# Performance work log

Hardware: AMD Instinct MI355X
Metric: run time of the kernel (lower is better)

Reference implementation:

```python
import jax, jax.numpy as jnp
import numpy as np


def _block(x, W, b, use_relu):
    # x: (B, n, dx). Faithful to PairwiseInteractions: full pairwise L2 dist,
    # top-k (k == n) smallest sorted, drop self, concat(self, neighbor), linear,
    # optional relu, mean over the n-1 neighbors.
    B, n, dx = x.shape
    sq = jnp.sum(x * x, axis=-1)                                   # (B, n)
    d2 = sq[:, :, None] + sq[:, None, :] - 2.0 * jnp.einsum('bnd,bmd->bnm', x, x)
    dist = jnp.sqrt(jnp.maximum(d2, 0.0))                          # (B, n, n)
    _, idx = jax.lax.top_k(-dist, n)                               # ascending distances
    idx_nb = idx[:, :, 1:]                                         # drop self -> (B, n, n-1)
    nbr = jnp.take_along_axis(x[:, None, :, :], idx_nb[..., None], axis=2)  # (B, n, n-1, dx)
    self_rep = jnp.broadcast_to(x[:, :, None, :], nbr.shape)
    pairs = jnp.concatenate([self_rep, nbr], axis=-1)              # (B, n, n-1, 2*dx)
    h = pairs @ W + b
    if use_relu:
        h = jax.nn.relu(h)
    return jnp.sum(h, axis=2) / (n - 1)                            # (B, n, d_out)


def setup_inputs() -> dict:
    key = jax.random.key(0)
    ks = jax.random.split(key, 4)
    B, N, d = 2, 1024, 3

    def lin(k, fin, fout):
        kw, kb = jax.random.split(k)
        lim = 1.0 / np.sqrt(fin).astype(np.float32)
        W = jax.random.uniform(kw, (fin, fout), minval=-lim, maxval=lim, dtype=jnp.float32)
        b = jax.random.uniform(kb, (fout,), minval=-lim, maxval=lim, dtype=jnp.float32)
        return W, b

    W1, b1 = lin(ks[1], 2 * d, 32)
    W2, b2 = lin(ks[2], 2 * 32, 64)
    W3, b3 = lin(ks[3], 2 * 64, d)
    x = jax.random.normal(ks[0], (B, N * d), dtype=jnp.float32)
    return {"x": x, "W1": W1, "b1": b1, "W2": W2, "b2": b2, "W3": W3, "b3": b3}


def reference(x, W1, b1, W2, b2, W3, b3):
    B = x.shape[0]
    d = W3.shape[1]
    N = x.shape[1] // d
    h = x.reshape(B, N, d)
    h = _block(h, W1, b1, True)    # eb1: d -> 32, relu
    h = _block(h, W2, b2, True)    # eb2: 32 -> 64, relu
    h = _block(h, W3, b3, False)   # eb3: 64 -> d, no relu
    return h.reshape(B, N * d)
```

## Files before the change

### kernel.cpp

```cpp
#include <hip/hip_runtime.h>

#define NN 1024

__global__ __launch_bounds__(256) void k1_pair32_ac2(
    const float* __restrict__ x,  const float* __restrict__ W1, const float* __restrict__ b1,
    const float* __restrict__ W2, const float* __restrict__ b2,
    float* __restrict__ a2g, float* __restrict__ c2g)
{
    __shared__ float cbuf[8192];
    __shared__ float rowbuf[4][32];

    const int tid  = threadIdx.x;
    const int wave = tid >> 6, lane = tid & 63;
    const int blk  = blockIdx.x;

    const int i  = blk * 4 + wave;
    const int b  = i >> 10;
    const int il = i & 1023;
    const int js = lane >> 5, f = lane & 31;
    const float* xb = x + b * (NN * 3);

    const float xi0 = xb[il*3+0], xi1 = xb[il*3+1], xi2 = xb[il*3+2];
    const float a     = xi0*W1[0*32+f] + xi1*W1[1*32+f] + xi2*W1[2*32+f];
    const float cself = xi0*W1[3*32+f] + xi1*W1[4*32+f] + xi2*W1[5*32+f] + b1[f];

    float acc = 0.f;
    const int f2 = tid & 31, r0 = tid >> 5;
    const float w3f = W1[3*32+f2], w4f = W1[4*32+f2], w5f = W1[5*32+f2], bf = b1[f2];
    for (int tile = 0; tile < NN; tile += 256) {
        #pragma unroll 4
        for (int k = 0; k < 32; ++k) {
            int r = tile + r0 + k*8;
            float y0 = xb[r*3+0], y1 = xb[r*3+1], y2 = xb[r*3+2];
            cbuf[(r0 + k*8)*32 + f2] = y0*w3f + y1*w4f + y2*w5f + bf;
        }
        __syncthreads();
        #pragma unroll 8
        for (int jj = js; jj < 256; jj += 2)
            acc += fmaxf(a + cbuf[jj*32 + f], 0.f);
        __syncthreads();
    }
    acc += __shfl_xor(acc, 32);
    float res = (acc - fmaxf(a + cself, 0.f)) * (1.0f/1023.0f);
    if (js == 0) rowbuf[wave][f] = res;
    __syncthreads();

    float av = 0.f, cv = b2[lane];
    #pragma unroll
    for (int d = 0; d < 32; ++d) {
        float hv = rowbuf[wave][d];
        av += hv * W2[d*64 + lane];
        cv += hv * W2[(32 + d)*64 + lane];
    }
    a2g[i*64 + lane] = av;
    c2g[i*64 + lane] = cv;
}

__global__ __launch_bounds__(256) void k2_pair64(
    const float* __restrict__ a2g, const float* __restrict__ c2g,
    float* __restrict__ out2, float* __restrict__ partials)
{
    __shared__ float cbuf[8192];
    __shared__ float pcol[4][64];

    const int tid  = threadIdx.x;
    const int wave = tid >> 6, lane = tid & 63;
    const int blk  = blockIdx.x;

    const int i = blk * 4 + wave;
    const int b = i >> 10;
    const float* cb = c2g + b * (NN * 64);
    const float a = a2g[i*64 + lane];
    float acc = 0.f;
    for (int tile = 0; tile < NN; tile += 128) {
        const float4* src = (const float4*)(cb + tile * 64);
        float4* dst = (float4*)cbuf;
        for (int k = tid; k < 2048; k += 256) dst[k] = src[k];
        __syncthreads();
        #pragma unroll 8
        for (int jj = 0; jj < 128; ++jj)
            acc += fmaxf(a + cbuf[jj*64 + lane], 0.f);
        __syncthreads();
    }
    float res = (acc - fmaxf(a + cb[(i & 1023)*64 + lane], 0.f)) * (1.0f/1023.0f);
    out2[i*64 + lane] = res;
    pcol[wave][lane] = res;
    __syncthreads();
    if (tid < 64)
        partials[blk*64 + tid] = pcol[0][tid] + pcol[1][tid] + pcol[2][tid] + pcol[3][tid];
}

__global__ __launch_bounds__(256) void k3_final(
    const float* __restrict__ out2, const float* __restrict__ partials,
    const float* __restrict__ W3, const float* __restrict__ b3,
    float* __restrict__ out)
{
    __shared__ float pcol[4][64];
    __shared__ float sS[4];

    const int tid  = threadIdx.x;
    const int wave = tid >> 6, lane = tid & 63;
    const int blk  = blockIdx.x;
    const int b = blk >> 2;

    {
        int col = tid & 63, q = tid >> 6;
        float s = 0.f;
        const float* pb = partials + b * 256 * 64;
        #pragma unroll 8
        for (int k = q*64; k < q*64 + 64; ++k) s += pb[k*64 + col];
        pcol[q][col] = s;
    }
    __syncthreads();
    if (wave < 3) {
        float cs = pcol[0][lane] + pcol[1][lane] + pcol[2][lane] + pcol[3][lane];
        float p = cs * W3[(64 + lane)*3 + wave];
        #pragma unroll
        for (int off = 32; off; off >>= 1) p += __shfl_xor(p, off);
        if (lane == 0) sS[wave] = p;
    }
    __syncthreads();

    const int t = blk * 256 + tid;
    const float* row = out2 + t * 64;
    float r0 = 0, r1 = 0, r2 = 0, q0 = 0, q1 = 0, q2 = 0;
    #pragma unroll
    for (int d = 0; d < 64; ++d) {
        float v = row[d];
        r0 += v * W3[d*3+0];       r1 += v * W3[d*3+1];       r2 += v * W3[d*3+2];
        q0 += v * W3[(64+d)*3+0];  q1 += v * W3[(64+d)*3+1];  q2 += v * W3[(64+d)*3+2];
    }
    float* o = out + t * 3;
    o[0] = r0 + b3[0] + (sS[0] - q0) * (1.0f/1023.0f);
    o[1] = r1 + b3[1] + (sS[1] - q1) * (1.0f/1023.0f);
    o[2] = r2 + b3[2] + (sS[2] - q2) * (1.0f/1023.0f);
}

extern "C" void kernel_launch(void* const* d_in, const int* in_sizes, int n_in,
                              void* d_out, int out_size, void* d_ws, size_t ws_size,
                              hipStream_t stream) {
    const float* x  = (const float*)d_in[0];
    const float* W1 = (const float*)d_in[1];
    const float* b1 = (const float*)d_in[2];
    const float* W2 = (const float*)d_in[3];
    const float* b2 = (const float*)d_in[4];
    const float* W3 = (const float*)d_in[5];
    const float* b3 = (const float*)d_in[6];
    float* out = (float*)d_out;

    float* ws = (float*)d_ws;
    float* a2g      = ws;
    float* c2g      = a2g  + 2048*64;
    float* out2     = c2g  + 2048*64;
    float* partials = out2 + 2048*64;

    k1_pair32_ac2<<<512, 256, 0, stream>>>(x, W1, b1, W2, b2, a2g, c2g);
    k2_pair64<<<512, 256, 0, stream>>>(a2g, c2g, out2, partials);
    k3_final<<<8, 256, 0, stream>>>(out2, partials, W3, b3, out);
}
```

Baseline: 114.5 us.

## Fuse layer-3 projection into pair64 kernel and register-block two rows per wave

The pair64 kernel now has each wave handle two rows over half of the neighbor columns, so each shared-memory load of c is reused for two accumulations. Partial sums are combined through shared memory. The final linear projection through W3 is folded into this kernel using wave shuffles, so the 64-wide intermediate is no longer written and re-read. The last kernel only reduces the 3-wide partial column sums and adds them to the output. This removes global traffic and most of the work in the final kernel, at the cost of extra shuffles and a read-modify-write on the output.

```diff
diff --git a/kernel.cpp b/kernel.cpp
--- a/kernel.cpp
+++ b/kernel.cpp
@@ -56,84 +56,101 @@
     c2g[i*64 + lane] = cv;
 }
 
-__global__ __launch_bounds__(256) void k2_pair64(
+__global__ __launch_bounds__(256) void k2_pair64_final(
     const float* __restrict__ a2g, const float* __restrict__ c2g,
-    float* __restrict__ out2, float* __restrict__ partials)
+    const float* __restrict__ W3, const float* __restrict__ b3,
+    float* __restrict__ out, float* __restrict__ partials)
 {
     __shared__ float cbuf[8192];
-    __shared__ float pcol[4][64];
+    __shared__ float pacc[4][2][64];
+    __shared__ float qpart[4][3];
 
     const int tid  = threadIdx.x;
     const int wave = tid >> 6, lane = tid & 63;
     const int blk  = blockIdx.x;
 
-    const int i = blk * 4 + wave;
-    const int b = i >> 10;
+    const int i0 = blk * 4;
+    const int b  = blk >> 8;
+    const int rw = wave >> 1, jh = wave & 1;
+    const int rowA = i0 + 2*rw, rowB = rowA + 1;
+
     const float* cb = c2g + b * (NN * 64);
-    const float a = a2g[i*64 + lane];
-    float acc = 0.f;
+    const float a0 = a2g[rowA*64 + lane];
+    const float a1 = a2g[rowB*64 + lane];
+    float acc0 = 0.f, acc1 = 0.f;
+
     for (int tile = 0; tile < NN; tile += 128) {
         const float4* src = (const float4*)(cb + tile * 64);
         float4* dst = (float4*)cbuf;
         for (int k = tid; k < 2048; k += 256) dst[k] = src[k];
         __syncthreads();
         #pragma unroll 8
-        for (int jj = 0; jj < 128; ++jj)
-            acc += fmaxf(a + cbuf[jj*64 + lane], 0.f);
+        for (int k = 0; k < 64; ++k) {
+            float c = cbuf[(2*k + jh)*64 + lane];
+            acc0 += fmaxf(a0 + c, 0.f);
+            acc1 += fmaxf(a1 + c, 0.f);
+        }
         __syncthreads();
     }
-    float res = (acc - fmaxf(a + cb[(i & 1023)*64 + lane], 0.f)) * (1.0f/1023.0f);
-    out2[i*64 + lane] = res;
-    pcol[wave][lane] = res;
+    pacc[wave][0][lane] = acc0;
+    pacc[wave][1][lane] = acc1;
     __syncthreads();
-    if (tid < 64)
-        partials[blk*64 + tid] = pcol[0][tid] + pcol[1][tid] + pcol[2][tid] + pcol[3][tid];
+
+    const int i = i0 + wave;
+    const int wpair = 2*(wave >> 1);
+    float accf = pacc[wpair][wave & 1][lane] + pacc[wpair + 1][wave & 1][lane];
+    float aself = a2g[i*64 + lane];
+    float self  = fmaxf(aself + cb[(i & 1023)*64 + lane], 0.f);
+    float res = (accf - self) * (1.0f/1023.0f);
+
+    float wt0 = W3[lane*3+0], wt1 = W3[lane*3+1], wt2 = W3[lane*3+2];
+    float wb0 = W3[(64+lane)*3+0], wb1 = W3[(64+lane)*3+1], wb2 = W3[(64+lane)*3+2];
+    float y0 = res * (wt0 - wb0*(1.0f/1023.0f));
+    float y1 = res * (wt1 - wb1*(1.0f/1023.0f));
+    float y2 = res * (wt2 - wb2*(1.0f/1023.0f));
+    float q0 = res * wb0, q1 = res * wb1, q2 = res * wb2;
+    #pragma unroll
+    for (int off = 32; off; off >>= 1) {
+        y0 += __shfl_xor(y0, off);  y1 += __shfl_xor(y1, off);  y2 += __shfl_xor(y2, off);
+        q0 += __shfl_xor(q0, off);  q1 += __shfl_xor(q1, off);  q2 += __shfl_xor(q2, off);
+    }
+    if (lane == 0) {
+        out[i*3+0] = y0 + b3[0];
+        out[i*3+1] = y1 + b3[1];
+        out[i*3+2] = y2 + b3[2];
+        qpart[wave][0] = q0;  qpart[wave][1] = q1;  qpart[wave][2] = q2;
+    }
+    __syncthreads();
+    if (tid < 3)
+        partials[blk*3 + tid] = qpart[0][tid] + qpart[1][tid] + qpart[2][tid] + qpart[3][tid];
 }
 
 __global__ __launch_bounds__(256) void k3_final(
-    const float* __restrict__ out2, const float* __restrict__ partials,
-    const float* __restrict__ W3, const float* __restrict__ b3,
-    float* __restrict__ out)
+    const float* __restrict__ partials, float* __restrict__ out)
 {
-    __shared__ float pcol[4][64];
-    __shared__ float sS[4];
+    __shared__ float red[4][3];
 
     const int tid  = threadIdx.x;
     const int wave = tid >> 6, lane = tid & 63;
     const int blk  = blockIdx.x;
     const int b = blk >> 2;
 
-    {
-        int col = tid & 63, q = tid >> 6;
-        float s = 0.f;
-        const float* pb = partials + b * 256 * 64;
-        #pragma unroll 8
-        for (int k = q*64; k < q*64 + 64; ++k) s += pb[k*64 + col];
-        pcol[q][col] = s;
+    const float* pb = partials + b * 256 * 3;
+    float s0 = pb[tid*3+0], s1 = pb[tid*3+1], s2 = pb[tid*3+2];
+    #pragma unroll
+    for (int off = 32; off; off >>= 1) {
+        s0 += __shfl_xor(s0, off);  s1 += __shfl_xor(s1, off);  s2 += __shfl_xor(s2, off);
     }
+    if (lane == 0) { red[wave][0] = s0; red[wave][1] = s1; red[wave][2] = s2; }
     __syncthreads();
-    if (wave < 3) {
-        float cs = pcol[0][lane] + pcol[1][lane] + pcol[2][lane] + pcol[3][lane];
-        float p = cs * W3[(64 + lane)*3 + wave];
-        #pragma unroll
-        for (int off = 32; off; off >>= 1) p += __shfl_xor(p, off);
-        if (lane == 0) sS[wave] = p;
-    }
-    __syncthreads();
+    float S0 = (red[0][0]+red[1][0]+red[2][0]+red[3][0]) * (1.0f/1023.0f);
+    float S1 = (red[0][1]+red[1][1]+red[2][1]+red[3][1]) * (1.0f/1023.0f);
+    float S2 = (red[0][2]+red[1][2]+red[2][2]+red[3][2]) * (1.0f/1023.0f);
 
-    const int t = blk * 256 + tid;
-    const float* row = out2 + t * 64;
-    float r0 = 0, r1 = 0, r2 = 0, q0 = 0, q1 = 0, q2 = 0;
-    #pragma unroll
-    for (int d = 0; d < 64; ++d) {
-        float v = row[d];
-        r0 += v * W3[d*3+0];       r1 += v * W3[d*3+1];       r2 += v * W3[d*3+2];
-        q0 += v * W3[(64+d)*3+0];  q1 += v * W3[(64+d)*3+1];  q2 += v * W3[(64+d)*3+2];
-    }
-    float* o = out + t * 3;
-    o[0] = r0 + b3[0] + (sS[0] - q0) * (1.0f/1023.0f);
-    o[1] = r1 + b3[1] + (sS[1] - q1) * (1.0f/1023.0f);
-    o[2] = r2 + b3[2] + (sS[2] - q2) * (1.0f/1023.0f);
+    const int i = b * NN + (blk & 3) * 256 + tid;
+    out[i*3+0] += S0;
+    out[i*3+1] += S1;
+    out[i*3+2] += S2;
 }
 
 extern "C" void kernel_launch(void* const* d_in, const int* in_sizes, int n_in,
@@ -150,11 +167,10 @@
 
     float* ws = (float*)d_ws;
     float* a2g      = ws;
-    float* c2g      = a2g  + 2048*64;
-    float* out2     = c2g  + 2048*64;
-    float* partials = out2 + 2048*64;
+    float* c2g      = a2g + 2048*64;
+    float* partials = c2g + 2048*64;
 
     k1_pair32_ac2<<<512, 256, 0, stream>>>(x, W1, b1, W2, b2, a2g, c2g);
-    k2_pair64<<<512, 256, 0, stream>>>(a2g, c2g, out2, partials);
-    k3_final<<<8, 256, 0, stream>>>(out2, partials, W3, b3, out);
+    k2_pair64_final<<<512, 256, 0, stream>>>(a2g, c2g, W3, b3, out, partials);
+    k3_final<<<8, 256, 0, stream>>>(partials, out);
 }
```

Result: faster. 105.3 us (-8.1%).
